# Kernel optimization log

Measured on AMD Instinct MI355X. Metric: run time of the kernel, lower is better.

Reference implementation:

```python
import jax, jax.numpy as jnp
import numpy as np

B, CIN, H, W = 8, 64, 128, 128
COUT, KH, KW = 64, 3, 3
STRIDE, PAD, DIL = 1, 1, 1
HO, WO = 128, 128


def setup_inputs() -> dict:
    key = jax.random.key(0)
    k1, k2, k3 = jax.random.split(key, 3)
    x = jax.random.normal(k1, (B, CIN, H, W), dtype=jnp.float32)
    offset = jax.random.normal(k2, (B, 2 * KH * KW, HO, WO), dtype=jnp.float32)
    fan_in = CIN * KH * KW
    weight = jax.random.normal(k3, (COUT, CIN, KH, KW), dtype=jnp.float32) / np.sqrt(fan_in)
    return {"x": x, "offset": offset, "weight": weight}


def _deform_conv(x, offset, weight):
    b, c, h, w = x.shape
    cout, cin, kh, kw = weight.shape
    k2 = kh * kw
    ho, wo = offset.shape[2], offset.shape[3]
    # offsets: interleaved (dy, dx) per kernel tap
    off = offset.reshape(b, k2, 2, ho, wo)
    dy, dx = off[:, :, 0], off[:, :, 1]                      # [B, K2, Ho, Wo]
    ky = jnp.repeat(jnp.arange(kh), kw).astype(x.dtype)       # [K2]
    kx = jnp.tile(jnp.arange(kw), kh).astype(x.dtype)
    base_y = (jnp.arange(ho) * STRIDE - PAD).astype(x.dtype)  # [Ho]
    base_x = (jnp.arange(wo) * STRIDE - PAD).astype(x.dtype)  # [Wo]
    py = dy + ky[None, :, None, None] * DIL + base_y[None, None, :, None]
    px = dx + kx[None, :, None, None] * DIL + base_x[None, None, None, :]

    y0 = jnp.floor(py)
    x0 = jnp.floor(px)
    wy1 = py - y0
    wx1 = px - x0
    y0i = y0.astype(jnp.int32)
    x0i = x0.astype(jnp.int32)

    def gather_corner(yi, xi, wgt):
        # zero-padding semantics: mask out-of-bounds corners
        valid = ((yi >= 0) & (yi < h) & (xi >= 0) & (xi < w)).astype(x.dtype)
        yc = jnp.clip(yi, 0, h - 1)
        xc = jnp.clip(xi, 0, w - 1)
        def per_batch(xb, yb, xbid, vb, wb):
            return xb[:, yb, xbid] * (vb * wb)[None]          # [C, K2, Ho, Wo]
        return jax.vmap(per_batch)(x, yc, xc, valid, wgt)

    # accumulate 4 corners to avoid holding all gathers at once
    sampled = gather_corner(y0i, x0i, (1 - wy1) * (1 - wx1))
    sampled = sampled + gather_corner(y0i, x0i + 1, (1 - wy1) * wx1)
    sampled = sampled + gather_corner(y0i + 1, x0i, wy1 * (1 - wx1))
    sampled = sampled + gather_corner(y0i + 1, x0i + 1, wy1 * wx1)
    # sampled: [B, Cin, K2, Ho, Wo]; conv-accumulate
    return jnp.einsum('bckhw,ock->bohw', sampled, weight.reshape(cout, cin, k2))


def reference(x, offset, weight):
    return _deform_conv(x, offset, weight)
```

## Files before the change

kernel.cpp:

```cpp
#include <hip/hip_runtime.h>
#include <hip/hip_bf16.h>

#define CIN  64
#define HH   128
#define WW   128
#define COUT 64
#define K2   9
#define HW   (HH * WW)

typedef __attribute__((ext_vector_type(8))) short bf16x8;
typedef __attribute__((ext_vector_type(4))) float f32x4;
typedef __attribute__((ext_vector_type(2))) float f32x2;
typedef __attribute__((ext_vector_type(4))) unsigned short u16x4;

__device__ __forceinline__ unsigned short f2bf(float f) {
    __hip_bfloat16 h = __float2bfloat16(f);
    return *reinterpret_cast<unsigned short*>(&h);
}
__device__ __forceinline__ f32x2 up2(unsigned int d) {
    f32x2 r;
    r[0] = __uint_as_float(d << 16);
    r[1] = __uint_as_float(d & 0xffff0000u);
    return r;
}

__launch_bounds__(256)
__global__ void xprep2_kernel(const float* __restrict__ x, unsigned short* __restrict__ xt) {
    const int idx = blockIdx.x * 256 + threadIdx.x;
    const int xw = idx & 127;
    const int y  = (idx >> 7) & 127;
    const int s  = (idx >> 14) & 7;
    const int b  = idx >> 17;
    const float* src = x + (((size_t)(b * CIN + s * 8) * HH) + y) * WW + xw;
    union { unsigned short us[8]; bf16x8 v; } u;
    #pragma unroll
    for (int j = 0; j < 8; ++j) u.us[j] = f2bf(src[(size_t)j * HW]);
    *(bf16x8*)(xt + ((((size_t)b * 8 + s) * HW) + y * WW + xw) * 8) = u.v;
}

__global__ void wprep_kernel(const float* __restrict__ w, unsigned short* __restrict__ wtp) {
    int idx = blockIdx.x * 256 + threadIdx.x;
    if (idx >= COUT * CIN * K2) return;
    int j  = idx & 7;
    int l  = (idx >> 3) & 63;
    int nt = (idx >> 9) & 3;
    int ks = (idx >> 11) & 1;
    int k  = idx >> 12;
    int o  = nt * 16 + (l & 15);
    int c  = ks * 32 + (l >> 4) * 8 + j;
    wtp[idx] = f2bf(w[(o * CIN + c) * K2 + k]);
}

__launch_bounds__(512, 4)
__global__ void dcn_kernel(const unsigned short* __restrict__ xt,
                           const float* __restrict__ off,
                           const unsigned short* __restrict__ wtp,
                           float* __restrict__ out) {
    __shared__ float sred[64][66];

    const int tid = threadIdx.x;
    const int w   = tid >> 6;
    const int l   = tid & 63;
    const int wr  = w & 3;
    const int wh  = w >> 2;

    int bid = blockIdx.x;
    bid = (bid & 7) * 256 + (bid >> 3);
    const int b   = bid >> 8;
    const int t   = bid & 255;
    const int ty0 = (t >> 3) << 2;
    const int tx0 = (t & 7) << 4;

    const int g      = l >> 4;
    const int lane16 = l & 15;

    f32x4 acc[4] = {{0,0,0,0},{0,0,0,0},{0,0,0,0},{0,0,0,0}};

    const float* offb = off + (size_t)b * (2 * K2) * HW;
    const unsigned short* xb  = xt + (size_t)b * HW * 64;
    const unsigned short* xp0 = xb + (size_t)g * HW * 8;
    const unsigned short* xp1 = xb + (size_t)(g + 4) * HW * 8;

    const int ypA  = ty0 + wr;
    const int xpA  = tx0 + lane16;
    const int offp = ypA * WW + xpA;

    f32x4 Pw[2];
    int   Pr0[2], Pr1[2];
    float oyv[2], oxv[2];
    bf16x8 G00L, G00R, G01L, G01R;
    bf16x8 G10L, G10R, G11L, G11R;
    bf16x8 bvv[2][4];
    bf16x8 af0, af1;

#define PARAMS(K, S) do {                                                     \
    const int kdy = (K) / 3 - 1, kdx = (K) % 3 - 1;                           \
    float py = oyv[S] + (float)(ypA + kdy);                                   \
    float px = oxv[S] + (float)(xpA + kdx);                                   \
    float fy = floorf(py), fx = floorf(px);                                   \
    float wy = py - fy, wxn = px - fx;                                        \
    int y0 = (int)fy, x0i = (int)fx;                                          \
    int yc0 = min(max(y0,     0), HH - 1);                                    \
    int yc1 = min(max(y0 + 1, 0), HH - 1);                                    \
    float ay0 = (y0 >= 0  && y0 <= HH - 1) ? (1.f - wy) : 0.f;                \
    float ay1 = (y0 >= -1 && y0 <= HH - 2) ? wy         : 0.f;                \
    int   xL  = min(max(x0i, 0), WW - 2);                                     \
    float bx0 = (x0i >= 0  && x0i <= WW - 1) ? (1.f - wxn) : 0.f;             \
    float bx1 = (x0i >= -1 && x0i <= WW - 2) ? wxn         : 0.f;             \
    bool  sw  = (x0i != xL);                                                  \
    float wxa = sw ? bx1 : bx0;                                               \
    float wxb = sw ? bx0 : bx1;                                               \
    Pw[S][0] = ay0 * wxa; Pw[S][1] = ay0 * wxb;                               \
    Pw[S][2] = ay1 * wxa; Pw[S][3] = ay1 * wxb;                               \
    Pr0[S] = (yc0 * WW + xL) * 8;                                             \
    Pr1[S] = (yc1 * WW + xL) * 8;                                             \
} while (0)

#define GATHER(S) do {                                                        \
    const unsigned short* r0p = xp0 + Pr0[S];                                 \
    const unsigned short* r1p = xp0 + Pr1[S];                                 \
    const unsigned short* r2p = xp1 + Pr0[S];                                 \
    const unsigned short* r3p = xp1 + Pr1[S];                                 \
    G00L = *(const bf16x8*)(r0p); G00R = *(const bf16x8*)(r0p + 8);           \
    G01L = *(const bf16x8*)(r1p); G01R = *(const bf16x8*)(r1p + 8);           \
    G10L = *(const bf16x8*)(r2p); G10R = *(const bf16x8*)(r2p + 8);           \
    G11L = *(const bf16x8*)(r3p); G11R = *(const bf16x8*)(r3p + 8);           \
} while (0)

#define IN1(S, GA, GB, GC, GD, AF) do {                                       \
    union { bf16x8 v; unsigned int d[4]; } ua, ub, uc, ud;                    \
    ua.v = GA; ub.v = GB; uc.v = GC; ud.v = GD;                               \
    union { unsigned short us[8]; bf16x8 v; } rr;                             \
    _Pragma("unroll")                                                         \
    for (int q = 0; q < 4; ++q) {                                             \
        f32x2 v = up2(ua.d[q]) * Pw[S][0] + up2(ub.d[q]) * Pw[S][1]           \
                + up2(uc.d[q]) * Pw[S][2] + up2(ud.d[q]) * Pw[S][3];          \
        rr.us[2*q]   = f2bf(v[0]);                                            \
        rr.us[2*q+1] = f2bf(v[1]);                                            \
    }                                                                         \
    AF = rr.v;                                                                \
} while (0)

#define INTERP(S) do {                                                        \
    IN1(S, G00L, G00R, G01L, G01R, af0);                                      \
    IN1(S, G10L, G10R, G11L, G11R, af1);                                      \
} while (0)

#define BVLOAD(K) do {                                                        \
    _Pragma("unroll")                                                         \
    for (int ks = 0; ks < 2; ++ks)                                            \
        _Pragma("unroll")                                                     \
        for (int nt = 0; nt < 4; ++nt)                                        \
            bvv[ks][nt] = *(const bf16x8*)(wtp + ((((K)*2 + ks)*4 + nt)*64 + l)*8); \
} while (0)

#define DOMFMA() do {                                                         \
    __builtin_amdgcn_s_setprio(1);                                            \
    _Pragma("unroll")                                                         \
    for (int nt = 0; nt < 4; ++nt)                                            \
        acc[nt] = __builtin_amdgcn_mfma_f32_16x16x32_bf16(af0, bvv[0][nt], acc[nt], 0, 0, 0); \
    _Pragma("unroll")                                                         \
    for (int nt = 0; nt < 4; ++nt)                                            \
        acc[nt] = __builtin_amdgcn_mfma_f32_16x16x32_bf16(af1, bvv[1][nt], acc[nt], 0, 0, 0); \
    __builtin_amdgcn_s_setprio(0);                                            \
} while (0)

#define STEP(K, CUR, NXT, KMAX) do {                                          \
    PARAMS((K) + 1, NXT);                                                     \
    if ((K) + 2 <= (KMAX)) {                                                  \
        oyv[CUR] = offb[(2 * ((K) + 2)    ) * HW + offp];                     \
        oxv[CUR] = offb[(2 * ((K) + 2) + 1) * HW + offp];                     \
    }                                                                         \
    BVLOAD(K);                                                                \
    INTERP(CUR);                                                              \
    GATHER(NXT);                                                              \
    DOMFMA();                                                                 \
} while (0)

    if (wh == 0) {
        oyv[0] = offb[offp];          oxv[0] = offb[HW + offp];
        oyv[1] = offb[2 * HW + offp]; oxv[1] = offb[3 * HW + offp];
        PARAMS(0, 0);
        GATHER(0);
        STEP(0, 0, 1, 4); STEP(1, 1, 0, 4); STEP(2, 0, 1, 4); STEP(3, 1, 0, 4);
        BVLOAD(4); INTERP(0); DOMFMA();
    } else {
        oyv[0] = offb[10 * HW + offp]; oxv[0] = offb[11 * HW + offp];
        oyv[1] = offb[12 * HW + offp]; oxv[1] = offb[13 * HW + offp];
        PARAMS(5, 0);
        GATHER(0);
        STEP(5, 0, 1, 8); STEP(6, 1, 0, 8); STEP(7, 0, 1, 8);
        BVLOAD(8); INTERP(1); DOMFMA();
    }

#undef PARAMS
#undef GATHER
#undef IN1
#undef INTERP
#undef BVLOAD
#undef DOMFMA
#undef STEP

    const int rq = g * 4;
    if (wh == 0) {
        #pragma unroll
        for (int nt = 0; nt < 4; ++nt)
            #pragma unroll
            for (int j = 0; j < 4; ++j)
                sred[wr * 16 + rq + j][nt * 16 + lane16] = acc[nt][j];
    }
    __syncthreads();
    if (wh == 1) {
        #pragma unroll
        for (int nt = 0; nt < 4; ++nt) {
            f32x4 v;
            #pragma unroll
            for (int j = 0; j < 4; ++j)
                v[j] = sred[wr * 16 + rq + j][nt * 16 + lane16] + acc[nt][j];
            const int o  = nt * 16 + lane16;
            const int yy = ty0 + wr;
            const int xx = tx0 + rq;
            *(f32x4*)&out[(((size_t)b * COUT + o) * HH + yy) * WW + xx] = v;
        }
    }
}

__global__ void wprep_fb(const float* __restrict__ w, unsigned short* __restrict__ wt) {
    int idx = blockIdx.x * 256 + threadIdx.x;
    if (idx >= COUT * CIN * K2) return;
    int o = idx / (CIN * K2);
    int r = idx % (CIN * K2);
    int k = r / CIN;
    int c = r % CIN;
    wt[idx] = f2bf(w[o * (CIN * K2) + c * K2 + k]);
}

__launch_bounds__(256)
__global__ void dcn_fb(const float* __restrict__ x, const float* __restrict__ off,
                       const unsigned short* __restrict__ wt, float* __restrict__ out) {
    __shared__ unsigned short s_s[64 * 66];
    const int tid = threadIdx.x;
    const int w = tid >> 6, l = tid & 63;
    const int bid = blockIdx.x;
    const int b = bid >> 8, t = bid & 255;
    const int ty0 = (t >> 4) << 3, tx0 = (t & 15) << 3;
    const int iy = l >> 3, ix = l & 7;
    const int ypix = ty0 + iy, xpix = tx0 + ix;
    f32x4 acc[4] = {{0,0,0,0},{0,0,0,0},{0,0,0,0},{0,0,0,0}};
    const int c0w = w * 16;
    for (int k = 0; k < K2; ++k) {
        float dy = off[(((b * (2*K2)) + 2*k    ) * HH + ypix) * WW + xpix];
        float dx = off[(((b * (2*K2)) + 2*k + 1) * HH + ypix) * WW + xpix];
        float py = dy + (float)(k / 3 + ypix - 1);
        float px = dx + (float)(k % 3 + xpix - 1);
        float fy = floorf(py), fx = floorf(px);
        float wy = py - fy, wx = px - fx;
        int y0 = (int)fy, x0 = (int)fx;
        int yc0 = min(max(y0, 0), HH-1), yc1 = min(max(y0+1, 0), HH-1);
        float ay0 = (y0 >= 0 && y0 <= HH-1) ? (1.f-wy) : 0.f;
        float ay1 = (y0 >= -1 && y0 <= HH-2) ? wy : 0.f;
        int xL = min(max(x0, 0), WW-2);
        float bx0 = (x0 >= 0 && x0 <= WW-1) ? (1.f-wx) : 0.f;
        float bx1 = (x0 >= -1 && x0 <= WW-2) ? wx : 0.f;
        bool sw = (x0 != xL);
        float wxa = sw ? bx1 : bx0, wxb = sw ? bx0 : bx1;
        float W0x = ay0*wxa, W0y = ay0*wxb, W1x = ay1*wxa, W1y = ay1*wxb;
        const float* r0 = x + ((b * CIN + c0w) * HH + yc0) * WW + xL;
        const float* r1 = x + ((b * CIN + c0w) * HH + yc1) * WW + xL;
        unsigned short* sd = &s_s[l * 66 + c0w];
        #pragma unroll
        for (int cc = 0; cc < 16; ++cc) {
            sd[cc] = f2bf(W0x*r0[0] + W0y*r0[1] + W1x*r1[0] + W1y*r1[1]);
            r0 += HH*WW; r1 += HH*WW;
        }
        __syncthreads();
        const int o_lane = l & 15, q = l >> 4;
        #pragma unroll
        for (int ks = 0; ks < 2; ++ks) {
            const int cb = ks*32 + q*8;
            const int row = w*16 + o_lane;
            const unsigned int* sp = (const unsigned int*)s_s;
            const int ib = row*33 + (cb >> 1);
            union { unsigned int u[4]; bf16x8 v; } af;
            af.u[0]=sp[ib]; af.u[1]=sp[ib+1]; af.u[2]=sp[ib+2]; af.u[3]=sp[ib+3];
            #pragma unroll
            for (int nt = 0; nt < 4; ++nt) {
                bf16x8 bfv = *(const bf16x8*)(wt + (nt*16 + o_lane) * (CIN*K2) + k*64 + cb);
                acc[nt] = __builtin_amdgcn_mfma_f32_16x16x32_bf16(af.v, bfv, acc[nt], 0, 0, 0);
            }
        }
        __syncthreads();
    }
    const int o_lane = l & 15, rq = (l >> 4) * 4;
    #pragma unroll
    for (int nt = 0; nt < 4; ++nt) {
        const int o = nt*16 + o_lane;
        #pragma unroll
        for (int j = 0; j < 4; ++j) {
            const int pix = w*16 + rq + j;
            out[(((size_t)b * COUT + o) * HH + ty0 + (pix>>3)) * WW + tx0 + (pix&7)] = acc[nt][j];
        }
    }
}

extern "C" void kernel_launch(void* const* d_in, const int* in_sizes, int n_in,
                              void* d_out, int out_size, void* d_ws, size_t ws_size,
                              hipStream_t stream) {
    const float* x   = (const float*)d_in[0];
    const float* off = (const float*)d_in[1];
    const float* wgt = (const float*)d_in[2];
    float* out = (float*)d_out;

    const size_t xt_bytes = (size_t)8 * HW * 64 * sizeof(unsigned short);
    const size_t wt_bytes = (size_t)COUT * CIN * K2 * sizeof(unsigned short);

    if (ws_size >= xt_bytes + wt_bytes) {
        unsigned short* xt  = (unsigned short*)d_ws;
        unsigned short* wtp = (unsigned short*)((char*)d_ws + xt_bytes);
        xprep2_kernel<<<4096, 256, 0, stream>>>(x, xt);
        wprep_kernel<<<(COUT * CIN * K2 + 255) / 256, 256, 0, stream>>>(wgt, wtp);
        dcn_kernel<<<2048, 512, 0, stream>>>(xt, off, wtp, out);
    } else {
        unsigned short* wt = (unsigned short*)d_ws;
        wprep_fb<<<(COUT * CIN * K2 + 255) / 256, 256, 0, stream>>>(wgt, wt);
        dcn_fb<<<2048, 256, 0, stream>>>(x, off, wt, out);
    }
}
```

Measured before the change: 68.43 us.

## Split channel halves across wave groups and stage weights through LDS

```diff
diff --git a/kernel.cpp b/kernel.cpp
--- a/kernel.cpp
+++ b/kernel.cpp
@@ -11,7 +11,6 @@
 typedef __attribute__((ext_vector_type(8))) short bf16x8;
 typedef __attribute__((ext_vector_type(4))) float f32x4;
 typedef __attribute__((ext_vector_type(2))) float f32x2;
-typedef __attribute__((ext_vector_type(4))) unsigned short u16x4;
 
 __device__ __forceinline__ unsigned short f2bf(float f) {
     __hip_bfloat16 h = __float2bfloat16(f);
@@ -22,6 +21,11 @@
     r[0] = __uint_as_float(d << 16);
     r[1] = __uint_as_float(d & 0xffff0000u);
     return r;
+}
+__device__ __forceinline__ void gl2lds16(const unsigned short* g, unsigned short* l) {
+    __builtin_amdgcn_global_load_lds(
+        (const __attribute__((address_space(1))) unsigned int*)g,
+        (__attribute__((address_space(3))) unsigned int*)l, 16, 0, 0);
 }
 
 __launch_bounds__(256)
@@ -56,6 +60,7 @@
                            const float* __restrict__ off,
                            const unsigned short* __restrict__ wtp,
                            float* __restrict__ out) {
+    __shared__ unsigned short lsB[2][4096];
     __shared__ float sred[64][66];
 
     const int tid = threadIdx.x;
@@ -77,9 +82,7 @@
     f32x4 acc[4] = {{0,0,0,0},{0,0,0,0},{0,0,0,0},{0,0,0,0}};
 
     const float* offb = off + (size_t)b * (2 * K2) * HW;
-    const unsigned short* xb  = xt + (size_t)b * HW * 64;
-    const unsigned short* xp0 = xb + (size_t)g * HW * 8;
-    const unsigned short* xp1 = xb + (size_t)(g + 4) * HW * 8;
+    const unsigned short* xp = xt + ((size_t)b * 8 + (wh * 4 + g)) * HW * 8;
 
     const int ypA  = ty0 + wr;
     const int xpA  = tx0 + lane16;
@@ -88,10 +91,9 @@
     f32x4 Pw[2];
     int   Pr0[2], Pr1[2];
     float oyv[2], oxv[2];
-    bf16x8 G00L, G00R, G01L, G01R;
-    bf16x8 G10L, G10R, G11L, G11R;
-    bf16x8 bvv[2][4];
-    bf16x8 af0, af1;
+    bf16x8 Gst[2][4];
+    bf16x8 bvv[4];
+    bf16x8 af;
 
 #define PARAMS(K, S) do {                                                     \
     const int kdy = (K) / 3 - 1, kdx = (K) % 3 - 1;                           \
@@ -117,19 +119,15 @@
 } while (0)
 
 #define GATHER(S) do {                                                        \
-    const unsigned short* r0p = xp0 + Pr0[S];                                 \
-    const unsigned short* r1p = xp0 + Pr1[S];                                 \
-    const unsigned short* r2p = xp1 + Pr0[S];                                 \
-    const unsigned short* r3p = xp1 + Pr1[S];                                 \
-    G00L = *(const bf16x8*)(r0p); G00R = *(const bf16x8*)(r0p + 8);           \
-    G01L = *(const bf16x8*)(r1p); G01R = *(const bf16x8*)(r1p + 8);           \
-    G10L = *(const bf16x8*)(r2p); G10R = *(const bf16x8*)(r2p + 8);           \
-    G11L = *(const bf16x8*)(r3p); G11R = *(const bf16x8*)(r3p + 8);           \
-} while (0)
-
-#define IN1(S, GA, GB, GC, GD, AF) do {                                       \
+    const unsigned short* r0p = xp + Pr0[S];                                  \
+    const unsigned short* r1p = xp + Pr1[S];                                  \
+    Gst[S][0] = *(const bf16x8*)(r0p); Gst[S][1] = *(const bf16x8*)(r0p + 8); \
+    Gst[S][2] = *(const bf16x8*)(r1p); Gst[S][3] = *(const bf16x8*)(r1p + 8); \
+} while (0)
+
+#define INTERP(S) do {                                                        \
     union { bf16x8 v; unsigned int d[4]; } ua, ub, uc, ud;                    \
-    ua.v = GA; ub.v = GB; uc.v = GC; ud.v = GD;                               \
+    ua.v = Gst[S][0]; ub.v = Gst[S][1]; uc.v = Gst[S][2]; ud.v = Gst[S][3];   \
     union { unsigned short us[8]; bf16x8 v; } rr;                             \
     _Pragma("unroll")                                                         \
     for (int q = 0; q < 4; ++q) {                                             \
@@ -138,68 +136,58 @@
         rr.us[2*q]   = f2bf(v[0]);                                            \
         rr.us[2*q+1] = f2bf(v[1]);                                            \
     }                                                                         \
-    AF = rr.v;                                                                \
-} while (0)
-
-#define INTERP(S) do {                                                        \
-    IN1(S, G00L, G00R, G01L, G01R, af0);                                      \
-    IN1(S, G10L, G10R, G11L, G11R, af1);                                      \
-} while (0)
-
-#define BVLOAD(K) do {                                                        \
+    af = rr.v;                                                                \
+} while (0)
+
+#define BVLOAD(P) do {                                                        \
     _Pragma("unroll")                                                         \
-    for (int ks = 0; ks < 2; ++ks)                                            \
-        _Pragma("unroll")                                                     \
-        for (int nt = 0; nt < 4; ++nt)                                        \
-            bvv[ks][nt] = *(const bf16x8*)(wtp + ((((K)*2 + ks)*4 + nt)*64 + l)*8); \
+    for (int nt = 0; nt < 4; ++nt)                                            \
+        bvv[nt] = *(const bf16x8*)(&lsB[P][(wh * 4 + nt) * 512 + l * 8]);     \
+} while (0)
+
+#define STAGE(P, K) do {                                                      \
+    gl2lds16(wtp + (K) * 4096 + w * 512 + l * 8, &lsB[P][w * 512]);           \
 } while (0)
 
 #define DOMFMA() do {                                                         \
     __builtin_amdgcn_s_setprio(1);                                            \
     _Pragma("unroll")                                                         \
     for (int nt = 0; nt < 4; ++nt)                                            \
-        acc[nt] = __builtin_amdgcn_mfma_f32_16x16x32_bf16(af0, bvv[0][nt], acc[nt], 0, 0, 0); \
-    _Pragma("unroll")                                                         \
-    for (int nt = 0; nt < 4; ++nt)                                            \
-        acc[nt] = __builtin_amdgcn_mfma_f32_16x16x32_bf16(af1, bvv[1][nt], acc[nt], 0, 0, 0); \
+        acc[nt] = __builtin_amdgcn_mfma_f32_16x16x32_bf16(af, bvv[nt], acc[nt], 0, 0, 0); \
     __builtin_amdgcn_s_setprio(0);                                            \
 } while (0)
 
-#define STEP(K, CUR, NXT, KMAX) do {                                          \
-    PARAMS((K) + 1, NXT);                                                     \
-    if ((K) + 2 <= (KMAX)) {                                                  \
-        oyv[CUR] = offb[(2 * ((K) + 2)    ) * HW + offp];                     \
-        oxv[CUR] = offb[(2 * ((K) + 2) + 1) * HW + offp];                     \
-    }                                                                         \
-    BVLOAD(K);                                                                \
-    INTERP(CUR);                                                              \
-    GATHER(NXT);                                                              \
-    DOMFMA();                                                                 \
-} while (0)
-
-    if (wh == 0) {
-        oyv[0] = offb[offp];          oxv[0] = offb[HW + offp];
-        oyv[1] = offb[2 * HW + offp]; oxv[1] = offb[3 * HW + offp];
-        PARAMS(0, 0);
-        GATHER(0);
-        STEP(0, 0, 1, 4); STEP(1, 1, 0, 4); STEP(2, 0, 1, 4); STEP(3, 1, 0, 4);
-        BVLOAD(4); INTERP(0); DOMFMA();
-    } else {
-        oyv[0] = offb[10 * HW + offp]; oxv[0] = offb[11 * HW + offp];
-        oyv[1] = offb[12 * HW + offp]; oxv[1] = offb[13 * HW + offp];
-        PARAMS(5, 0);
-        GATHER(0);
-        STEP(5, 0, 1, 8); STEP(6, 1, 0, 8); STEP(7, 0, 1, 8);
-        BVLOAD(8); INTERP(1); DOMFMA();
+    STAGE(0, 0);
+    oyv[0] = offb[offp];          oxv[0] = offb[HW + offp];
+    oyv[1] = offb[2 * HW + offp]; oxv[1] = offb[3 * HW + offp];
+    PARAMS(0, 0);
+    GATHER(0);
+    __syncthreads();
+
+    #pragma unroll
+    for (int s = 0; s < K2; ++s) {
+        const int cur = s & 1, nxt = cur ^ 1;
+        if (s < 8) {
+            STAGE(nxt, s + 1);
+            PARAMS(s + 1, nxt);
+            if (s < 7) {
+                oyv[cur] = offb[(2 * (s + 2)    ) * HW + offp];
+                oxv[cur] = offb[(2 * (s + 2) + 1) * HW + offp];
+            }
+            GATHER(nxt);
+        }
+        BVLOAD(cur);
+        INTERP(cur);
+        DOMFMA();
+        if (s < 8) __syncthreads();
     }
 
 #undef PARAMS
 #undef GATHER
-#undef IN1
 #undef INTERP
 #undef BVLOAD
+#undef STAGE
 #undef DOMFMA
-#undef STEP
 
     const int rq = g * 4;
     if (wh == 0) {
```

Measured after the change: 62.20 us. 9.1% less time.
